# Kernel tuning notes

Hardware: AMD Instinct MI355X
Metric: run time of the kernel (lower is better)

Reference implementation:

```python
import jax, jax.numpy as jnp
import numpy as np

H = 256; HEADS = 4; DH = H // HEADS; LAYERS = 2; FEAT = 7
N = 20000; L = 32; E = 640000


def _ln(x, g, b, eps=1e-5):
    mu = x.mean(-1, keepdims=True)
    var = ((x - mu) ** 2).mean(-1, keepdims=True)
    return (x - mu) / jnp.sqrt(var + eps) * g + b


def setup_inputs() -> dict:
    key = jax.random.key(0)
    ks = jax.random.split(key, 12)
    s = 0.05
    nrm = lambda k, shp: jax.random.normal(k, shp, jnp.float32) * s
    return {
        "literal_reprs": jax.random.normal(ks[0], (N, L, H), jnp.float32),
        "clause_features": jax.random.uniform(ks[1], (N, FEAT), jnp.float32),
        "mask": jax.random.randint(ks[2], (N, L), 0, 2) == 1,
        "adjacency": jax.random.randint(ks[3], (2, E), 0, N),
        "pe_w1": nrm(ks[4], (FEAT, H)), "pe_b1": jnp.zeros((H,), jnp.float32),
        "pe_w2": nrm(ks[5], (H, H)), "pe_b2": jnp.zeros((H,), jnp.float32),
        "attn_in_w": nrm(ks[6], (H, 3 * H)), "attn_in_b": jnp.zeros((3 * H,), jnp.float32),
        "attn_out_w": nrm(ks[7], (H, H)), "attn_out_b": jnp.zeros((H,), jnp.float32),
        "attn_ln_g": jnp.ones((H,), jnp.float32), "attn_ln_b": jnp.zeros((H,), jnp.float32),
        "gate_w": nrm(ks[8], (2 * H, H)), "gate_b": jnp.zeros((H,), jnp.float32),
        "trans_w": nrm(ks[9], (2 * H, H)), "trans_b": jnp.zeros((H,), jnp.float32),
        "fus_ln_g": jnp.ones((H,), jnp.float32), "fus_ln_b": jnp.zeros((H,), jnp.float32),
        "mp_w": nrm(ks[10], (LAYERS, 2 * H, H)), "mp_b": jnp.zeros((LAYERS, H), jnp.float32),
        "mp_ln_g": jnp.ones((LAYERS, H), jnp.float32), "mp_ln_b": jnp.zeros((LAYERS, H), jnp.float32),
    }


def reference(literal_reprs, clause_features, mask, adjacency,
              pe_w1, pe_b1, pe_w2, pe_b2,
              attn_in_w, attn_in_b, attn_out_w, attn_out_b,
              attn_ln_g, attn_ln_b, gate_w, gate_b, trans_w, trans_b,
              fus_ln_g, fus_ln_b, mp_w, mp_b, mp_ln_g, mp_ln_b):
    n, l, h = literal_reprs.shape
    # clause property encoder (shared by query and fusion path)
    enc = jnp.maximum(clause_features @ pe_w1 + pe_b1, 0.0) @ pe_w2 + pe_b2  # (N, H)
    # single-query multi-head attention over literals
    wq, wk, wv = attn_in_w[:, :H], attn_in_w[:, H:2 * H], attn_in_w[:, 2 * H:]
    bq, bk, bv = attn_in_b[:H], attn_in_b[H:2 * H], attn_in_b[2 * H:]
    q = ((enc @ wq + bq) * (1.0 / np.sqrt(DH))).reshape(n, HEADS, DH)
    k = (literal_reprs @ wk + bk).reshape(n, l, HEADS, DH)
    v = (literal_reprs @ wv + bv).reshape(n, l, HEADS, DH)
    scores = jnp.einsum('nhd,nlhd->nhl', q, k)
    kpm = ~mask  # True = masked out
    all_masked = jnp.all(kpm, axis=1)
    kpm = kpm.at[:, 0].set(jnp.where(all_masked, False, kpm[:, 0]))  # unmask pos 0 for fully-masked rows
    scores = jnp.where(kpm[:, None, :], -jnp.inf, scores)
    attn = jax.nn.softmax(scores, axis=-1)
    ctx = jnp.einsum('nhl,nlhd->nhd', attn, v).reshape(n, h) @ attn_out_w + attn_out_b
    ctx = jnp.where(all_masked[:, None], 0.0, ctx)  # zero fully-masked rows
    attn_repr = _ln(ctx + enc, attn_ln_g, attn_ln_b)
    # masked mean-pool residual
    mf = mask.astype(literal_reprs.dtype)[:, :, None]
    lit_mean = (literal_reprs * mf).sum(1) / jnp.maximum(mf.sum(1), 1.0)
    attn_repr = attn_repr + lit_mean
    # gated fusion
    combined = jnp.concatenate([attn_repr, enc], axis=-1)
    gate = jax.nn.sigmoid(combined @ gate_w + gate_b)
    transform = combined @ trans_w + trans_b
    x = _ln(gate * attn_repr + (1.0 - gate) * transform, fus_ln_g, fus_ln_b)
    # inter-clause message passing
    src, dst = adjacency[0], adjacency[1]
    ones = jnp.ones((src.shape[0],), x.dtype)
    for i in range(LAYERS):
        agg = jax.ops.segment_sum(x[src], dst, num_segments=n)
        cnt = jax.ops.segment_sum(ones, dst, num_segments=n)
        agg = agg / jnp.maximum(cnt, 1.0)[:, None]
        upd = jnp.maximum(jnp.concatenate([x, agg], axis=-1) @ mp_w[i] + mp_b[i], 0.0)
        x = _ln(x + upd, mp_ln_g[i], mp_ln_b[i])
    return x
```

## Files before the change

### kernel.cpp

```cpp
#include <hip/hip_runtime.h>
#include <math.h>

#define H 256
#define L 32
#define HEADS 4
#define FEAT 7
#define LN_EPS 1e-5f

typedef __attribute__((ext_vector_type(8))) short bf16x8;
typedef __attribute__((ext_vector_type(4))) float f32x4;

__device__ __forceinline__ float wave_reduce_sum64(float v) {
#pragma unroll
  for (int m = 32; m >= 1; m >>= 1) v += __shfl_xor(v, m, 64);
  return v;
}

__device__ __forceinline__ short bf16rne(float f) {
  unsigned u = __float_as_uint(f);
  unsigned r = (u + 0x7FFFu + ((u >> 16) & 1u)) >> 16;
  return (short)r;
}

__device__ __forceinline__ float bf2f(short s) {
  return __uint_as_float(((unsigned)(unsigned short)s) << 16);
}

__global__ __launch_bounds__(256) void k_pack_w(
    const float* __restrict__ W, short* __restrict__ P, int K, int N) {
  const int KS = K / 32;
  const int total = (N / 16) * KS * 64;
  int t = blockIdx.x * 256 + threadIdx.x;
  if (t >= total) return;
  const int lane = t & 63;
  const int ks = (t >> 6) % KS;
  const int tcol = (t >> 6) / KS;
  const int j = tcol * 16 + (lane & 15);
  const int k0 = ks * 32 + (lane >> 4) * 8;
  short v[8];
#pragma unroll
  for (int i = 0; i < 8; ++i) v[i] = bf16rne(W[(size_t)(k0 + i) * N + j]);
  *(int4*)&P[(size_t)t * 8] = *(int4*)v;
}

__global__ __launch_bounds__(256) void k_pack_w4(
    const float* __restrict__ w0, const float* __restrict__ w1,
    const float* __restrict__ w2, const float* __restrict__ w3,
    short* __restrict__ p0, short* __restrict__ p1,
    short* __restrict__ p2, short* __restrict__ p3) {
  const float* W = (blockIdx.y == 0) ? w0 : (blockIdx.y == 1) ? w1 : (blockIdx.y == 2) ? w2 : w3;
  short* P = (blockIdx.y == 0) ? p0 : (blockIdx.y == 1) ? p1 : (blockIdx.y == 2) ? p2 : p3;
  const int KS = 16;
  int t = blockIdx.x * 256 + threadIdx.x;
  const int lane = t & 63;
  const int ks = (t >> 6) % KS;
  const int tcol = (t >> 6) / KS;
  const int j = tcol * 16 + (lane & 15);
  const int k0 = ks * 32 + (lane >> 4) * 8;
  short v[8];
#pragma unroll
  for (int i = 0; i < 8; ++i) v[i] = bf16rne(W[(size_t)(k0 + i) * 256 + j]);
  *(int4*)&P[(size_t)t * 8] = *(int4*)v;
}

__global__ __launch_bounds__(256) void k_make_wqp(const float* __restrict__ aiw, short* __restrict__ P) {
  int t = blockIdx.x * 256 + threadIdx.x;
  const int lane = t & 63;
  const int ks = (t >> 6) & 7;
  const int tcol = t >> 9;
  const int col = tcol * 16 + (lane & 15);
  const int h = col >> 8, c = col & 255;
  const int k0 = ks * 32 + (lane >> 4) * 8;
  short v[8];
#pragma unroll
  for (int i = 0; i < 8; ++i) {
    const int k = k0 + i;
    float s = 0.f;
    for (int d = 0; d < 64; d += 4) {
      const float4 qa = *(const float4*)&aiw[(size_t)k * 768 + h * 64 + d];
      const float4 ka = *(const float4*)&aiw[(size_t)c * 768 + 256 + h * 64 + d];
      s = fmaf(qa.x, ka.x, fmaf(qa.y, ka.y, fmaf(qa.z, ka.z, fmaf(qa.w, ka.w, s))));
    }
    v[i] = bf16rne(0.125f * s);
  }
  *(int4*)&P[(size_t)t * 8] = *(int4*)v;
}

__global__ __launch_bounds__(256) void k_make_wbig(
    const float* __restrict__ aiw, const float* __restrict__ aow, short* __restrict__ P) {
  int t = blockIdx.x * 256 + threadIdx.x;
  const int lane = t & 63;
  const int ks = (t >> 6) & 31;
  const int tcol = t >> 11;
  const int j = tcol * 16 + (lane & 15);
  const int k0 = ks * 32 + (lane >> 4) * 8;
  short v[8];
#pragma unroll
  for (int i = 0; i < 8; ++i) {
    const int k = k0 + i;
    const int h = k >> 8, c = k & 255;
    float s = 0.f;
    for (int d = 0; d < 64; ++d)
      s = fmaf(aiw[(size_t)c * 768 + 512 + h * 64 + d], aow[(size_t)(h * 64 + d) * 256 + j], s);
    v[i] = bf16rne(s);
  }
  *(int4*)&P[(size_t)t * 8] = *(int4*)v;
}

__global__ void k_bias_p(const float* __restrict__ aiw, const float* __restrict__ aib,
                         float* __restrict__ bias_p) {
  const int col = threadIdx.x + blockIdx.x * 256;
  const int h = col >> 8, c = col & 255;
  float s = 0.f;
  for (int d = 0; d < 64; ++d)
    s = fmaf(aib[h * 64 + d], aiw[(size_t)c * 768 + 256 + h * 64 + d], s);
  bias_p[col] = 0.125f * s;
}

__global__ void k_bias_out(const float* __restrict__ aow, const float* __restrict__ aib,
                           const float* __restrict__ aob, float* __restrict__ bias_out) {
  const int j = threadIdx.x;
  float s = aob[j];
  for (int e = 0; e < 256; ++e) s = fmaf(aib[512 + e], aow[(size_t)e * 256 + j], s);
  bias_out[j] = s;
}

__global__ __launch_bounds__(256) void k_enc_mfma(
    const float* __restrict__ cf, const float* __restrict__ pe_w1, const float* __restrict__ pe_b1,
    const short* __restrict__ w2P, const float* __restrict__ pe_b2,
    const short* __restrict__ wqpP, const float* __restrict__ bias_p,
    short* __restrict__ enc_bf16, short* __restrict__ p_bf16, int n) {
  __shared__ float cfs[32][FEAT];
  __shared__ short h1[32][264];
  __shared__ short encS[32][264];
  const int tid = threadIdx.x;
  const int lane = tid & 63, w = tid >> 6;
  const int n0 = blockIdx.x * 32;
  for (int idx = tid; idx < 32 * FEAT; idx += 256) cfs[idx / FEAT][idx % FEAT] = cf[(size_t)n0 * FEAT + idx];
  __syncthreads();
  {
    const int j = tid;
    float wv[FEAT];
#pragma unroll
    for (int f = 0; f < FEAT; ++f) wv[f] = pe_w1[f * H + j];
    const float b1v = pe_b1[j];
    for (int r = 0; r < 32; ++r) {
      float s = b1v;
#pragma unroll
      for (int f = 0; f < FEAT; ++f) s = fmaf(cfs[r][f], wv[f], s);
      h1[r][j] = bf16rne(fmaxf(s, 0.f));
    }
  }
  __syncthreads();
  const int arow = lane & 15;
  const int koff = (lane >> 4) * 8;
  {
    f32x4 acc[2][4];
#pragma unroll
    for (int rt = 0; rt < 2; ++rt)
#pragma unroll
      for (int ct = 0; ct < 4; ++ct) acc[rt][ct] = (f32x4)0.f;
#pragma unroll
    for (int ks = 0; ks < 8; ++ks) {
      const int k0 = ks * 32 + koff;
      const bf16x8 a0 = *(const bf16x8*)&h1[arow][k0];
      const bf16x8 a1 = *(const bf16x8*)&h1[16 + arow][k0];
#pragma unroll
      for (int ct = 0; ct < 4; ++ct) {
        const size_t fo = (((size_t)(w * 4 + ct) * 8 + ks) * 64 + lane) * 8;
        const bf16x8 b = *(const bf16x8*)&w2P[fo];
        acc[0][ct] = __builtin_amdgcn_mfma_f32_16x16x32_bf16(a0, b, acc[0][ct], 0, 0, 0);
        acc[1][ct] = __builtin_amdgcn_mfma_f32_16x16x32_bf16(a1, b, acc[1][ct], 0, 0, 0);
      }
    }
#pragma unroll
    for (int rt = 0; rt < 2; ++rt)
#pragma unroll
      for (int ct = 0; ct < 4; ++ct) {
        const int col = w * 64 + ct * 16 + (lane & 15);
        const float b2v = pe_b2[col];
#pragma unroll
        for (int i = 0; i < 4; ++i) {
          const int row = rt * 16 + (lane >> 4) * 4 + i;
          const short bv = bf16rne(acc[rt][ct][i] + b2v);
          encS[row][col] = bv;
          enc_bf16[(size_t)(n0 + row) * H + col] = bv;
        }
      }
  }
  __syncthreads();
#pragma unroll
  for (int chunk = 0; chunk < 2; ++chunk) {
    f32x4 acc[2][8];
#pragma unroll
    for (int rt = 0; rt < 2; ++rt)
#pragma unroll
      for (int c8 = 0; c8 < 8; ++c8) acc[rt][c8] = (f32x4)0.f;
#pragma unroll
    for (int ks = 0; ks < 8; ++ks) {
      const int k0 = ks * 32 + koff;
      const bf16x8 a0 = *(const bf16x8*)&encS[arow][k0];
      const bf16x8 a1 = *(const bf16x8*)&encS[16 + arow][k0];
#pragma unroll
      for (int c8 = 0; c8 < 8; ++c8) {
        const int tcol = w * 16 + chunk * 8 + c8;
        const size_t fo = (((size_t)tcol * 8 + ks) * 64 + lane) * 8;
        const bf16x8 b = *(const bf16x8*)&wqpP[fo];
        acc[0][c8] = __builtin_amdgcn_mfma_f32_16x16x32_bf16(a0, b, acc[0][c8], 0, 0, 0);
        acc[1][c8] = __builtin_amdgcn_mfma_f32_16x16x32_bf16(a1, b, acc[1][c8], 0, 0, 0);
      }
    }
#pragma unroll
    for (int rt = 0; rt < 2; ++rt)
#pragma unroll
      for (int c8 = 0; c8 < 8; ++c8) {
        const int col = w * 256 + (chunk * 8 + c8) * 16 + (lane & 15);
        const float bp = bias_p[col];
#pragma unroll
        for (int i = 0; i < 4; ++i) {
          const int row = rt * 16 + (lane >> 4) * 4 + i;
          p_bf16[(size_t)(n0 + row) * 1024 + col] = bf16rne(acc[rt][c8][i] + bp);
        }
      }
  }
}

__global__ __launch_bounds__(256) void k_attn(
    const float* __restrict__ lit, const int* __restrict__ mask,
    const short* __restrict__ p_in, short* __restrict__ m_out,
    short* __restrict__ litmean_bf, int* __restrict__ flags, int n) {
  __shared__ short lit_bs[32][264];
  __shared__ float attn_s[32][4];
  __shared__ int validS[32];
  __shared__ int nvalidS;
  const int j = threadIdx.x;
  const int nn = blockIdx.x;
  const float* litrow = lit + (size_t)nn * (L * H);
  float lreg[32];
#pragma unroll
  for (int t = 0; t < 32; ++t) {
    const float v = litrow[t * 256 + j];
    lreg[t] = v;
    lit_bs[t][j] = bf16rne(v);
  }
  if (j < 32) validS[j] = (mask[(size_t)nn * L + j] != 0) ? 1 : 0;
  __syncthreads();
  if (j == 0) {
    int c = 0;
#pragma unroll
    for (int l = 0; l < 32; ++l) c += validS[l];
    nvalidS = c;
  }
  __syncthreads();
  const int nvalid = nvalidS;
  const bool allm = (nvalid == 0);
  if (j < 64) {
    const int lane = j;
    f32x4 sc0 = (f32x4)0.f, sc1 = (f32x4)0.f;
    const int hh = lane & 3;
    const int krow = (lane >> 4) * 8;
    const short* prow = p_in + (size_t)nn * 1024 + hh * 256;
#pragma unroll
    for (int ks = 0; ks < 8; ++ks) {
      const bf16x8 a = *(const bf16x8*)&prow[ks * 32 + krow];
      const bf16x8 b0 = *(const bf16x8*)&lit_bs[lane & 15][ks * 32 + krow];
      const bf16x8 b1 = *(const bf16x8*)&lit_bs[16 + (lane & 15)][ks * 32 + krow];
      sc0 = __builtin_amdgcn_mfma_f32_16x16x32_bf16(a, b0, sc0, 0, 0, 0);
      sc1 = __builtin_amdgcn_mfma_f32_16x16x32_bf16(a, b1, sc1, 0, 0, 0);
    }
    if (lane < 16) {
      const int l0 = lane, l1 = 16 + lane;
      const bool ok0 = validS[l0] || (allm && l0 == 0);
      const bool ok1 = validS[l1] != 0;
#pragma unroll
      for (int i = 0; i < 4; ++i) {
        float s0 = ok0 ? sc0[i] : -INFINITY;
        float s1 = ok1 ? sc1[i] : -INFINITY;
        float mx = fmaxf(s0, s1);
#pragma unroll
        for (int m = 8; m >= 1; m >>= 1) mx = fmaxf(mx, __shfl_xor(mx, m, 16));
        float e0 = ok0 ? __expf(s0 - mx) : 0.f;
        float e1 = ok1 ? __expf(s1 - mx) : 0.f;
        float sm = e0 + e1;
#pragma unroll
        for (int m = 8; m >= 1; m >>= 1) sm += __shfl_xor(sm, m, 16);
        const float inv = 1.f / sm;
        attn_s[l0][i] = e0 * inv;
        attn_s[l1][i] = e1 * inv;
      }
    }
  }
  __syncthreads();
  {
    const float inv = 1.f / fmaxf((float)nvalid, 1.f);
    float lm = 0.f;
#pragma unroll
    for (int l = 0; l < 32; ++l)
      if (validS[l]) lm += lreg[l];
    litmean_bf[(size_t)nn * H + j] = bf16rne(lm * inv);
    float mm0 = 0.f, mm1 = 0.f, mm2 = 0.f, mm3 = 0.f;
#pragma unroll
    for (int l = 0; l < 32; ++l) {
      const float4 av = *(const float4*)&attn_s[l][0];
      const float lv = lreg[l];
      mm0 = fmaf(av.x, lv, mm0);
      mm1 = fmaf(av.y, lv, mm1);
      mm2 = fmaf(av.z, lv, mm2);
      mm3 = fmaf(av.w, lv, mm3);
    }
    m_out[(size_t)nn * 1024 + 0 * 256 + j] = bf16rne(mm0);
    m_out[(size_t)nn * 1024 + 1 * 256 + j] = bf16rne(mm1);
    m_out[(size_t)nn * 1024 + 2 * 256 + j] = bf16rne(mm2);
    m_out[(size_t)nn * 1024 + 3 * 256 + j] = bf16rne(mm3);
  }
  if (j == 0) flags[nn] = allm ? 1 : 0;
}

__global__ __launch_bounds__(256) void k_fused(
    const short* __restrict__ m_bf16, const short* __restrict__ wbigP, const float* __restrict__ bias_out,
    const short* __restrict__ enc_bf16, const short* __restrict__ litmean_bf, const int* __restrict__ flags,
    const float* __restrict__ ag, const float* __restrict__ ab,
    const short* __restrict__ gwP, const short* __restrict__ twP,
    const float* __restrict__ gb, const float* __restrict__ tb,
    const float* __restrict__ fg, const float* __restrict__ fb,
    short* __restrict__ xout_bf, int n) {
  __shared__ short As[32][520];
  __shared__ float v_s[32][260];
  __shared__ float mu_s[32], sg_s[32];
  __shared__ int flagS[32];
  const int tid = threadIdx.x;
  const int lane = tid & 63, w = tid >> 6;
  const int n0 = blockIdx.x * 32;
  for (int q8 = tid; q8 < 32 * 32; q8 += 256) {
    const int idx = q8 << 3;
    const int r = idx >> 8, c = idx & 255;
    *(int4*)&As[r][256 + c] = *(const int4*)&enc_bf16[(size_t)(n0 + r) * H + c];
  }
  if (tid < 32) flagS[tid] = flags[n0 + tid];
  const int arow = lane & 15;
  const int koff = (lane >> 4) * 8;
  f32x4 acc[2][4];
#pragma unroll
  for (int rt = 0; rt < 2; ++rt)
#pragma unroll
    for (int ct = 0; ct < 4; ++ct) acc[rt][ct] = (f32x4)0.f;
#pragma unroll 8
  for (int ks = 0; ks < 32; ++ks) {
    const size_t abase = (size_t)(n0 + arow) * 1024 + ks * 32 + koff;
    const bf16x8 a0 = *(const bf16x8*)&m_bf16[abase];
    const bf16x8 a1 = *(const bf16x8*)&m_bf16[abase + 16 * 1024];
#pragma unroll
    for (int ct = 0; ct < 4; ++ct) {
      const size_t fo = (((size_t)(w * 4 + ct) * 32 + ks) * 64 + lane) * 8;
      const bf16x8 bw = *(const bf16x8*)&wbigP[fo];
      acc[0][ct] = __builtin_amdgcn_mfma_f32_16x16x32_bf16(a0, bw, acc[0][ct], 0, 0, 0);
      acc[1][ct] = __builtin_amdgcn_mfma_f32_16x16x32_bf16(a1, bw, acc[1][ct], 0, 0, 0);
    }
  }
  __syncthreads();
#pragma unroll
  for (int rt = 0; rt < 2; ++rt)
#pragma unroll
    for (int ct = 0; ct < 4; ++ct) {
      const int col = w * 64 + ct * 16 + (lane & 15);
      const float bo = bias_out[col];
#pragma unroll
      for (int i = 0; i < 4; ++i) {
        const int row = rt * 16 + (lane >> 4) * 4 + i;
        const float o = flagS[row] ? 0.f : (acc[rt][ct][i] + bo);
        v_s[row][col] = o + bf2f(As[row][256 + col]);
      }
    }
  __syncthreads();
  for (int r = w; r < 32; r += 4) {
    float ps = 0.f, pq = 0.f;
#pragma unroll
    for (int t = 0; t < 4; ++t) {
      float v = v_s[r][lane + 64 * t];
      ps += v;
      pq = fmaf(v, v, pq);
    }
    ps = wave_reduce_sum64(ps);
    pq = wave_reduce_sum64(pq);
    if (lane == 0) {
      float mu = ps * (1.f / H);
      mu_s[r] = mu;
      sg_s[r] = rsqrtf(pq * (1.f / H) - mu * mu + LN_EPS);
    }
  }
  __syncthreads();
  {
    const float agv = ag[tid], abv = ab[tid];
    for (int r = 0; r < 32; ++r) {
      const float val = (v_s[r][tid] - mu_s[r]) * sg_s[r] * agv + abv +
                        bf2f(litmean_bf[(size_t)(n0 + r) * H + tid]);
      As[r][tid] = bf16rne(val);
    }
  }
  __syncthreads();
  f32x4 accg[2][4], acct[2][4];
#pragma unroll
  for (int rt = 0; rt < 2; ++rt)
#pragma unroll
    for (int ct = 0; ct < 4; ++ct) { accg[rt][ct] = (f32x4)0.f; acct[rt][ct] = (f32x4)0.f; }
#pragma unroll 4
  for (int ks = 0; ks < 16; ++ks) {
    const int k0 = ks * 32 + koff;
    const bf16x8 a0 = *(const bf16x8*)&As[arow][k0];
    const bf16x8 a1 = *(const bf16x8*)&As[16 + arow][k0];
#pragma unroll
    for (int ct = 0; ct < 4; ++ct) {
      const size_t fo = (((size_t)(w * 4 + ct) * 16 + ks) * 64 + lane) * 8;
      const bf16x8 bg = *(const bf16x8*)&gwP[fo];
      const bf16x8 bt = *(const bf16x8*)&twP[fo];
      accg[0][ct] = __builtin_amdgcn_mfma_f32_16x16x32_bf16(a0, bg, accg[0][ct], 0, 0, 0);
      accg[1][ct] = __builtin_amdgcn_mfma_f32_16x16x32_bf16(a1, bg, accg[1][ct], 0, 0, 0);
      acct[0][ct] = __builtin_amdgcn_mfma_f32_16x16x32_bf16(a0, bt, acct[0][ct], 0, 0, 0);
      acct[1][ct] = __builtin_amdgcn_mfma_f32_16x16x32_bf16(a1, bt, acct[1][ct], 0, 0, 0);
    }
  }
#pragma unroll
  for (int rt = 0; rt < 2; ++rt)
#pragma unroll
    for (int ct = 0; ct < 4; ++ct) {
      const int col = w * 64 + ct * 16 + (lane & 15);
      const float gbv = gb[col], tbv = tb[col];
#pragma unroll
      for (int i = 0; i < 4; ++i) {
        const int rl = rt * 16 + (lane >> 4) * 4 + i;
        const float gate = 1.f / (1.f + __expf(-(accg[rt][ct][i] + gbv)));
        const float tr = acct[rt][ct][i] + tbv;
        const float a = bf2f(As[rl][col]);
        v_s[rl][col] = fmaf(gate, a - tr, tr);
      }
    }
  __syncthreads();
  for (int r = w; r < 32; r += 4) {
    float ps = 0.f, pq = 0.f;
#pragma unroll
    for (int t = 0; t < 4; ++t) {
      float v = v_s[r][lane + 64 * t];
      ps += v;
      pq = fmaf(v, v, pq);
    }
    ps = wave_reduce_sum64(ps);
    pq = wave_reduce_sum64(pq);
    if (lane == 0) {
      float mu = ps * (1.f / H);
      mu_s[r] = mu;
      sg_s[r] = rsqrtf(pq * (1.f / H) - mu * mu + LN_EPS);
    }
  }
  __syncthreads();
  {
    const float fgv = fg[tid], fbv = fb[tid];
    for (int r = 0; r < 32; ++r)
      xout_bf[(size_t)(n0 + r) * H + tid] = bf16rne((v_s[r][tid] - mu_s[r]) * sg_s[r] * fgv + fbv);
  }
}

__global__ __launch_bounds__(256) void k_mp_mfma(
    const short* __restrict__ xin_bf, const short* __restrict__ agg_bf,
    const short* __restrict__ wP, const float* __restrict__ bias,
    const float* __restrict__ g, const float* __restrict__ b,
    float* __restrict__ xout_f32, short* __restrict__ xout_bf, int n) {
  __shared__ short As[32][520];
  __shared__ float v_s[32][260];
  __shared__ float mu_s[32], sg_s[32];
  const int tid = threadIdx.x;
  const int lane = tid & 63, w = tid >> 6;
  const int n0 = blockIdx.x * 32;
  for (int q8 = tid; q8 < 32 * 64; q8 += 256) {
    const int idx = q8 << 3;
    const int r = idx >> 9, c = idx & 511;
    const short* src = (c < H) ? &xin_bf[(size_t)(n0 + r) * H + c]
                               : &agg_bf[(size_t)(n0 + r) * H + (c - H)];
    *(int4*)&As[r][c] = *(const int4*)src;
  }
  __syncthreads();
  f32x4 acc[2][4];
#pragma unroll
  for (int rt = 0; rt < 2; ++rt)
#pragma unroll
    for (int ct = 0; ct < 4; ++ct) acc[rt][ct] = (f32x4)0.f;
  const int arow = lane & 15;
  const int koff = (lane >> 4) * 8;
#pragma unroll 4
  for (int ks = 0; ks < 16; ++ks) {
    const int k0 = ks * 32 + koff;
    const bf16x8 a0 = *(const bf16x8*)&As[arow][k0];
    const bf16x8 a1 = *(const bf16x8*)&As[16 + arow][k0];
#pragma unroll
    for (int ct = 0; ct < 4; ++ct) {
      const size_t fo = (((size_t)(w * 4 + ct) * 16 + ks) * 64 + lane) * 8;
      const bf16x8 bw = *(const bf16x8*)&wP[fo];
      acc[0][ct] = __builtin_amdgcn_mfma_f32_16x16x32_bf16(a0, bw, acc[0][ct], 0, 0, 0);
      acc[1][ct] = __builtin_amdgcn_mfma_f32_16x16x32_bf16(a1, bw, acc[1][ct], 0, 0, 0);
    }
  }
#pragma unroll
  for (int rt = 0; rt < 2; ++rt)
#pragma unroll
    for (int ct = 0; ct < 4; ++ct) {
      const int col = w * 64 + ct * 16 + (lane & 15);
      const float bsv = bias[col];
#pragma unroll
      for (int i = 0; i < 4; ++i) {
        const int rl = rt * 16 + (lane >> 4) * 4 + i;
        const float u = fmaxf(acc[rt][ct][i] + bsv, 0.f);
        v_s[rl][col] = bf2f(As[rl][col]) + u;
      }
    }
  __syncthreads();
  for (int r = w; r < 32; r += 4) {
    float ps = 0.f, pq = 0.f;
#pragma unroll
    for (int t = 0; t < 4; ++t) {
      float v = v_s[r][lane + 64 * t];
      ps += v;
      pq = fmaf(v, v, pq);
    }
    ps = wave_reduce_sum64(ps);
    pq = wave_reduce_sum64(pq);
    if (lane == 0) {
      float mu = ps * (1.f / H);
      mu_s[r] = mu;
      sg_s[r] = rsqrtf(pq * (1.f / H) - mu * mu + LN_EPS);
    }
  }
  __syncthreads();
  const float gv = g[tid], bv = b[tid];
  for (int r = 0; r < 32; ++r) {
    const float val = (v_s[r][tid] - mu_s[r]) * sg_s[r] * gv + bv;
    if (xout_f32) xout_f32[(size_t)(n0 + r) * H + tid] = val;
    if (xout_bf) xout_bf[(size_t)(n0 + r) * H + tid] = bf16rne(val);
  }
}

__global__ void k_zero_int(int* __restrict__ p, int count) {
  int i = blockIdx.x * blockDim.x + threadIdx.x;
  if (i < count) p[i] = 0;
}

__global__ void k_hist(const int* __restrict__ dst, int* __restrict__ hist, int e) {
  int i = blockIdx.x * blockDim.x + threadIdx.x;
  if (i < e) atomicAdd(&hist[dst[i]], 1);
}

__global__ __launch_bounds__(1024) void k_scan(
    const int* __restrict__ hist, int* __restrict__ row_ptr, int* __restrict__ cursor, int n, int e) {
  __shared__ int part[1024];
  const int t = threadIdx.x;
  const int chunk = (n + 1023) / 1024;
  const int lo = t * chunk;
  const int hi = min(lo + chunk, n);
  int s = 0;
  for (int i = lo; i < hi; ++i) s += hist[i];
  part[t] = s;
  __syncthreads();
  for (int d = 1; d < 1024; d <<= 1) {
    int v = (t >= d) ? part[t - d] : 0;
    __syncthreads();
    part[t] += v;
    __syncthreads();
  }
  int run = (t > 0) ? part[t - 1] : 0;
  for (int i = lo; i < hi; ++i) {
    row_ptr[i] = run;
    cursor[i] = run;
    run += hist[i];
  }
  if (t == 1023) row_ptr[n] = e;
}

__global__ void k_fill(const int* __restrict__ adj, int* __restrict__ cursor,
                       int* __restrict__ edge_src, int e) {
  int i = blockIdx.x * blockDim.x + threadIdx.x;
  if (i < e) {
    int s = adj[i], d = adj[e + i];
    int pos = atomicAdd(&cursor[d], 1);
    edge_src[pos] = s;
  }
}

__global__ __launch_bounds__(256) void k_gather(
    const short* __restrict__ x, const int* __restrict__ edge_src, const int* __restrict__ row_ptr,
    short* __restrict__ agg, int n) {
  const int wid = threadIdx.x >> 6;
  const int lane = threadIdx.x & 63;
  const int d = blockIdx.x * 4 + wid;
  if (d >= n) return;
  const int beg = row_ptr[d], end = row_ptr[d + 1];
  float4 acc = {0.f, 0.f, 0.f, 0.f};
  int i = beg;
  for (; i + 4 <= end; i += 4) {
    const int s0 = edge_src[i], s1 = edge_src[i + 1], s2 = edge_src[i + 2], s3 = edge_src[i + 3];
    const short4 v0 = *(const short4*)(x + (size_t)s0 * H + lane * 4);
    const short4 v1 = *(const short4*)(x + (size_t)s1 * H + lane * 4);
    const short4 v2 = *(const short4*)(x + (size_t)s2 * H + lane * 4);
    const short4 v3 = *(const short4*)(x + (size_t)s3 * H + lane * 4);
    acc.x += bf2f(v0.x) + bf2f(v1.x) + bf2f(v2.x) + bf2f(v3.x);
    acc.y += bf2f(v0.y) + bf2f(v1.y) + bf2f(v2.y) + bf2f(v3.y);
    acc.z += bf2f(v0.z) + bf2f(v1.z) + bf2f(v2.z) + bf2f(v3.z);
    acc.w += bf2f(v0.w) + bf2f(v1.w) + bf2f(v2.w) + bf2f(v3.w);
  }
  for (; i < end; ++i) {
    const int s = edge_src[i];
    const short4 v = *(const short4*)(x + (size_t)s * H + lane * 4);
    acc.x += bf2f(v.x); acc.y += bf2f(v.y); acc.z += bf2f(v.z); acc.w += bf2f(v.w);
  }
  const float inv = 1.f / fmaxf((float)(end - beg), 1.f);
  short4 o;
  o.x = bf16rne(acc.x * inv); o.y = bf16rne(acc.y * inv);
  o.z = bf16rne(acc.z * inv); o.w = bf16rne(acc.w * inv);
  *(short4*)(agg + (size_t)d * H + lane * 4) = o;
}

extern "C" void kernel_launch(void* const* d_in, const int* in_sizes, int n_in,
                              void* d_out, int out_size, void* d_ws, size_t ws_size,
                              hipStream_t stream) {
  const float* lit = (const float*)d_in[0];
  const float* cf = (const float*)d_in[1];
  const int* mask = (const int*)d_in[2];
  const int* adj = (const int*)d_in[3];
  const float* pe_w1 = (const float*)d_in[4];
  const float* pe_b1 = (const float*)d_in[5];
  const float* pe_w2 = (const float*)d_in[6];
  const float* pe_b2 = (const float*)d_in[7];
  const float* aiw = (const float*)d_in[8];
  const float* aib = (const float*)d_in[9];
  const float* aow = (const float*)d_in[10];
  const float* aob = (const float*)d_in[11];
  const float* attn_ln_g = (const float*)d_in[12];
  const float* attn_ln_b = (const float*)d_in[13];
  const float* gate_w = (const float*)d_in[14];
  const float* gate_b = (const float*)d_in[15];
  const float* trans_w = (const float*)d_in[16];
  const float* trans_b = (const float*)d_in[17];
  const float* fus_ln_g = (const float*)d_in[18];
  const float* fus_ln_b = (const float*)d_in[19];
  const float* mp_w = (const float*)d_in[20];
  const float* mp_b = (const float*)d_in[21];
  const float* mp_ln_g = (const float*)d_in[22];
  const float* mp_ln_b = (const float*)d_in[23];

  const int n = in_sizes[1] / FEAT;
  const int e = in_sizes[3] / 2;

  float* ws = (float*)d_ws;
  size_t off = 0;
  short* enc_bf16 = (short*)(ws + off); off += (size_t)n * 128;
  short* pm_bf16 = (short*)(ws + off); off += (size_t)n * 512;
  short* litmean_bf = (short*)(ws + off); off += (size_t)n * 128;
  short* x0_bf = (short*)(ws + off); off += (size_t)n * 128;
  short* x1_bf = (short*)(ws + off); off += (size_t)n * 128;
  short* agg_bf = (short*)(ws + off); off += (size_t)n * 128;
  int* flags = (int*)(ws + off); off += n;
  int* hist = (int*)(ws + off); off += n;
  int* row_ptr = (int*)(ws + off); off += n + 2;
  int* cursor = (int*)(ws + off); off += n;
  int* edge_src = (int*)(ws + off); off += e;
  short* w2P = (short*)(ws + off); off += 256 * 256 / 2;
  short* wqpP = (short*)(ws + off); off += 256 * 1024 / 2;
  short* wbigP = (short*)(ws + off); off += 1024 * 256 / 2;
  short* gwP = (short*)(ws + off); off += 512 * 256 / 2;
  short* twP = (short*)(ws + off); off += 512 * 256 / 2;
  short* mp0P = (short*)(ws + off); off += 512 * 256 / 2;
  short* mp1P = (short*)(ws + off); off += 512 * 256 / 2;
  float* bias_p = ws + off; off += 1024;
  float* bias_out = ws + off; off += 256;

  dim3 blk(256);
  k_pack_w<<<32, blk, 0, stream>>>(pe_w2, w2P, 256, 256);
  k_pack_w4<<<dim3(64, 4), blk, 0, stream>>>(gate_w, trans_w, mp_w, mp_w + 512 * 256,
                                             gwP, twP, mp0P, mp1P);
  k_make_wqp<<<128, blk, 0, stream>>>(aiw, wqpP);
  k_make_wbig<<<128, blk, 0, stream>>>(aiw, aow, wbigP);
  k_bias_p<<<4, blk, 0, stream>>>(aiw, aib, bias_p);
  k_bias_out<<<1, blk, 0, stream>>>(aow, aib, aob, bias_out);

  k_enc_mfma<<<n / 32, blk, 0, stream>>>(cf, pe_w1, pe_b1, w2P, pe_b2, wqpP, bias_p, enc_bf16, pm_bf16, n);
  k_attn<<<n, blk, 0, stream>>>(lit, mask, pm_bf16, pm_bf16, litmean_bf, flags, n);

  k_zero_int<<<(n + 255) / 256, blk, 0, stream>>>(hist, n);
  k_hist<<<(e + 255) / 256, blk, 0, stream>>>(adj + e, hist, e);
  k_scan<<<1, 1024, 0, stream>>>(hist, row_ptr, cursor, n, e);
  k_fill<<<(e + 255) / 256, blk, 0, stream>>>(adj, cursor, edge_src, e);

  k_fused<<<n / 32, blk, 0, stream>>>(pm_bf16, wbigP, bias_out, enc_bf16, litmean_bf, flags,
                                      attn_ln_g, attn_ln_b, gwP, twP, gate_b, trans_b,
                                      fus_ln_g, fus_ln_b, x0_bf, n);
  k_gather<<<(n + 3) / 4, blk, 0, stream>>>(x0_bf, edge_src, row_ptr, agg_bf, n);
  k_mp_mfma<<<n / 32, blk, 0, stream>>>(x0_bf, agg_bf, mp0P, mp_b, mp_ln_g, mp_ln_b,
                                        nullptr, x1_bf, n);
  k_gather<<<(n + 3) / 4, blk, 0, stream>>>(x1_bf, edge_src, row_ptr, agg_bf, n);
  k_mp_mfma<<<n / 32, blk, 0, stream>>>(x1_bf, agg_bf, mp1P, mp_b + 256, mp_ln_g + 256, mp_ln_b + 256,
                                        (float*)d_out, nullptr, n);
}
```

Baseline: 657.5 us.

## Fuse neighbor gather into MP GEMM, merge prep kernels, vectorize attention loads

The six weight-prep launches are merged into one block-dispatched k_prep kernel. The per-layer k_gather kernel is removed: each k_mp_mfma block now computes the mean over its rows' incoming neighbors straight into shared memory, which drops the agg buffer's global write and read. k_attn now loads literals as float4 into bf16 shared memory instead of keeping fp32 copies in registers. It also writes the per-head context vector interleaved (j*4+h) with a single short4 store, and the wbig packing layout is changed to match. The literal mean is now computed from bf16-rounded values, which slightly lowers its precision, and the fused gather puts irregular latency inside the GEMM blocks.

```diff
diff --git a/kernel.cpp b/kernel.cpp
--- a/kernel.cpp
+++ b/kernel.cpp
@@ -26,103 +26,93 @@
   return __uint_as_float(((unsigned)(unsigned short)s) << 16);
 }
 
-__global__ __launch_bounds__(256) void k_pack_w(
-    const float* __restrict__ W, short* __restrict__ P, int K, int N) {
-  const int KS = K / 32;
-  const int total = (N / 16) * KS * 64;
-  int t = blockIdx.x * 256 + threadIdx.x;
-  if (t >= total) return;
-  const int lane = t & 63;
-  const int ks = (t >> 6) % KS;
-  const int tcol = (t >> 6) / KS;
-  const int j = tcol * 16 + (lane & 15);
-  const int k0 = ks * 32 + (lane >> 4) * 8;
-  short v[8];
-#pragma unroll
-  for (int i = 0; i < 8; ++i) v[i] = bf16rne(W[(size_t)(k0 + i) * N + j]);
-  *(int4*)&P[(size_t)t * 8] = *(int4*)v;
-}
-
-__global__ __launch_bounds__(256) void k_pack_w4(
-    const float* __restrict__ w0, const float* __restrict__ w1,
-    const float* __restrict__ w2, const float* __restrict__ w3,
-    short* __restrict__ p0, short* __restrict__ p1,
-    short* __restrict__ p2, short* __restrict__ p3) {
-  const float* W = (blockIdx.y == 0) ? w0 : (blockIdx.y == 1) ? w1 : (blockIdx.y == 2) ? w2 : w3;
-  short* P = (blockIdx.y == 0) ? p0 : (blockIdx.y == 1) ? p1 : (blockIdx.y == 2) ? p2 : p3;
-  const int KS = 16;
-  int t = blockIdx.x * 256 + threadIdx.x;
-  const int lane = t & 63;
-  const int ks = (t >> 6) % KS;
-  const int tcol = (t >> 6) / KS;
-  const int j = tcol * 16 + (lane & 15);
-  const int k0 = ks * 32 + (lane >> 4) * 8;
-  short v[8];
-#pragma unroll
-  for (int i = 0; i < 8; ++i) v[i] = bf16rne(W[(size_t)(k0 + i) * 256 + j]);
-  *(int4*)&P[(size_t)t * 8] = *(int4*)v;
-}
-
-__global__ __launch_bounds__(256) void k_make_wqp(const float* __restrict__ aiw, short* __restrict__ P) {
-  int t = blockIdx.x * 256 + threadIdx.x;
-  const int lane = t & 63;
-  const int ks = (t >> 6) & 7;
-  const int tcol = t >> 9;
-  const int col = tcol * 16 + (lane & 15);
-  const int h = col >> 8, c = col & 255;
-  const int k0 = ks * 32 + (lane >> 4) * 8;
-  short v[8];
-#pragma unroll
-  for (int i = 0; i < 8; ++i) {
-    const int k = k0 + i;
-    float s = 0.f;
-    for (int d = 0; d < 64; d += 4) {
-      const float4 qa = *(const float4*)&aiw[(size_t)k * 768 + h * 64 + d];
-      const float4 ka = *(const float4*)&aiw[(size_t)c * 768 + 256 + h * 64 + d];
-      s = fmaf(qa.x, ka.x, fmaf(qa.y, ka.y, fmaf(qa.z, ka.z, fmaf(qa.w, ka.w, s))));
-    }
-    v[i] = bf16rne(0.125f * s);
-  }
-  *(int4*)&P[(size_t)t * 8] = *(int4*)v;
-}
-
-__global__ __launch_bounds__(256) void k_make_wbig(
-    const float* __restrict__ aiw, const float* __restrict__ aow, short* __restrict__ P) {
-  int t = blockIdx.x * 256 + threadIdx.x;
-  const int lane = t & 63;
-  const int ks = (t >> 6) & 31;
-  const int tcol = t >> 11;
-  const int j = tcol * 16 + (lane & 15);
-  const int k0 = ks * 32 + (lane >> 4) * 8;
-  short v[8];
-#pragma unroll
-  for (int i = 0; i < 8; ++i) {
-    const int k = k0 + i;
-    const int h = k >> 8, c = k & 255;
+__global__ __launch_bounds__(256) void k_prep(
+    const float* __restrict__ pe_w2, const float* __restrict__ aiw, const float* __restrict__ aow,
+    const float* __restrict__ aib, const float* __restrict__ aob,
+    const float* __restrict__ gate_w, const float* __restrict__ trans_w, const float* __restrict__ mp_w,
+    short* __restrict__ w2P, short* __restrict__ wqpP, short* __restrict__ wbigP,
+    short* __restrict__ gwP, short* __restrict__ twP, short* __restrict__ mp0P, short* __restrict__ mp1P,
+    float* __restrict__ bias_p, float* __restrict__ bias_out) {
+  const int bb = blockIdx.x;
+  const int tid = threadIdx.x;
+  if (bb < 32) {
+    const int t = bb * 256 + tid;
+    const int lane = t & 63;
+    const int ks = (t >> 6) & 7;
+    const int tcol = (t >> 6) >> 3;
+    const int j = tcol * 16 + (lane & 15);
+    const int k0 = ks * 32 + (lane >> 4) * 8;
+    short v[8];
+#pragma unroll
+    for (int i = 0; i < 8; ++i) v[i] = bf16rne(pe_w2[(size_t)(k0 + i) * 256 + j]);
+    *(int4*)&w2P[(size_t)t * 8] = *(int4*)v;
+  } else if (bb < 160) {
+    const int t = (bb - 32) * 256 + tid;
+    const int lane = t & 63;
+    const int ks = (t >> 6) & 7;
+    const int tcol = t >> 9;
+    const int col = tcol * 16 + (lane & 15);
+    const int h = col >> 8, c = col & 255;
+    const int k0 = ks * 32 + (lane >> 4) * 8;
+    short v[8];
+#pragma unroll
+    for (int i = 0; i < 8; ++i) {
+      const int k = k0 + i;
+      float s = 0.f;
+      for (int d = 0; d < 64; d += 4) {
+        const float4 qa = *(const float4*)&aiw[(size_t)k * 768 + h * 64 + d];
+        const float4 ka = *(const float4*)&aiw[(size_t)c * 768 + 256 + h * 64 + d];
+        s = fmaf(qa.x, ka.x, fmaf(qa.y, ka.y, fmaf(qa.z, ka.z, fmaf(qa.w, ka.w, s))));
+      }
+      v[i] = bf16rne(0.125f * s);
+    }
+    *(int4*)&wqpP[(size_t)t * 8] = *(int4*)v;
+  } else if (bb < 288) {
+    const int t = (bb - 160) * 256 + tid;
+    const int lane = t & 63;
+    const int ks = (t >> 6) & 31;
+    const int tcol = t >> 11;
+    const int j = tcol * 16 + (lane & 15);
+    const int k0 = ks * 32 + (lane >> 4) * 8;
+    short v[8];
+#pragma unroll
+    for (int i = 0; i < 8; ++i) {
+      const int k = k0 + i;
+      const int c = k >> 2, h = k & 3;
+      float s = 0.f;
+      for (int d = 0; d < 64; ++d)
+        s = fmaf(aiw[(size_t)c * 768 + 512 + h * 64 + d], aow[(size_t)(h * 64 + d) * 256 + j], s);
+      v[i] = bf16rne(s);
+    }
+    *(int4*)&wbigP[(size_t)t * 8] = *(int4*)v;
+  } else if (bb < 544) {
+    const int sub = bb - 288;
+    const int mi = sub >> 6;
+    const float* W = (mi == 0) ? gate_w : (mi == 1) ? trans_w : (mi == 2) ? mp_w : (mp_w + 512 * 256);
+    short* P = (mi == 0) ? gwP : (mi == 1) ? twP : (mi == 2) ? mp0P : mp1P;
+    const int t = (sub & 63) * 256 + tid;
+    const int lane = t & 63;
+    const int ks = (t >> 6) & 15;
+    const int tcol = (t >> 6) >> 4;
+    const int j = tcol * 16 + (lane & 15);
+    const int k0 = ks * 32 + (lane >> 4) * 8;
+    short v[8];
+#pragma unroll
+    for (int i = 0; i < 8; ++i) v[i] = bf16rne(W[(size_t)(k0 + i) * 256 + j]);
+    *(int4*)&P[(size_t)t * 8] = *(int4*)v;
+  } else if (bb < 548) {
+    const int col = (bb - 544) * 256 + tid;
+    const int h = col >> 8, c = col & 255;
     float s = 0.f;
     for (int d = 0; d < 64; ++d)
-      s = fmaf(aiw[(size_t)c * 768 + 512 + h * 64 + d], aow[(size_t)(h * 64 + d) * 256 + j], s);
-    v[i] = bf16rne(s);
-  }
-  *(int4*)&P[(size_t)t * 8] = *(int4*)v;
-}
-
-__global__ void k_bias_p(const float* __restrict__ aiw, const float* __restrict__ aib,
-                         float* __restrict__ bias_p) {
-  const int col = threadIdx.x + blockIdx.x * 256;
-  const int h = col >> 8, c = col & 255;
-  float s = 0.f;
-  for (int d = 0; d < 64; ++d)
-    s = fmaf(aib[h * 64 + d], aiw[(size_t)c * 768 + 256 + h * 64 + d], s);
-  bias_p[col] = 0.125f * s;
-}
-
-__global__ void k_bias_out(const float* __restrict__ aow, const float* __restrict__ aib,
-                           const float* __restrict__ aob, float* __restrict__ bias_out) {
-  const int j = threadIdx.x;
-  float s = aob[j];
-  for (int e = 0; e < 256; ++e) s = fmaf(aib[512 + e], aow[(size_t)e * 256 + j], s);
-  bias_out[j] = s;
+      s = fmaf(aib[h * 64 + d], aiw[(size_t)c * 768 + 256 + h * 64 + d], s);
+    bias_p[col] = 0.125f * s;
+  } else {
+    const int j = tid;
+    float s = aob[j];
+    for (int e2 = 0; e2 < 256; ++e2) s = fmaf(aib[512 + e2], aow[(size_t)e2 * 256 + j], s);
+    bias_out[j] = s;
+  }
 }
 
 __global__ __launch_bounds__(256) void k_enc_mfma(
@@ -236,12 +226,14 @@
   const int j = threadIdx.x;
   const int nn = blockIdx.x;
   const float* litrow = lit + (size_t)nn * (L * H);
-  float lreg[32];
-#pragma unroll
-  for (int t = 0; t < 32; ++t) {
-    const float v = litrow[t * 256 + j];
-    lreg[t] = v;
-    lit_bs[t][j] = bf16rne(v);
+#pragma unroll
+  for (int t = 0; t < 8; ++t) {
+    const int idx = (t * 256 + j) << 2;
+    const int r = idx >> 8, c = idx & 255;
+    const float4 f = *(const float4*)&litrow[idx];
+    short4 hv;
+    hv.x = bf16rne(f.x); hv.y = bf16rne(f.y); hv.z = bf16rne(f.z); hv.w = bf16rne(f.w);
+    *(short4*)&lit_bs[r][c] = hv;
   }
   if (j < 32) validS[j] = (mask[(size_t)nn * L + j] != 0) ? 1 : 0;
   __syncthreads();
@@ -294,24 +286,21 @@
   {
     const float inv = 1.f / fmaxf((float)nvalid, 1.f);
     float lm = 0.f;
-#pragma unroll
-    for (int l = 0; l < 32; ++l)
-      if (validS[l]) lm += lreg[l];
-    litmean_bf[(size_t)nn * H + j] = bf16rne(lm * inv);
     float mm0 = 0.f, mm1 = 0.f, mm2 = 0.f, mm3 = 0.f;
 #pragma unroll
     for (int l = 0; l < 32; ++l) {
+      const float lv = bf2f(lit_bs[l][j]);
+      if (validS[l]) lm += lv;
       const float4 av = *(const float4*)&attn_s[l][0];
-      const float lv = lreg[l];
       mm0 = fmaf(av.x, lv, mm0);
       mm1 = fmaf(av.y, lv, mm1);
       mm2 = fmaf(av.z, lv, mm2);
       mm3 = fmaf(av.w, lv, mm3);
     }
-    m_out[(size_t)nn * 1024 + 0 * 256 + j] = bf16rne(mm0);
-    m_out[(size_t)nn * 1024 + 1 * 256 + j] = bf16rne(mm1);
-    m_out[(size_t)nn * 1024 + 2 * 256 + j] = bf16rne(mm2);
-    m_out[(size_t)nn * 1024 + 3 * 256 + j] = bf16rne(mm3);
+    litmean_bf[(size_t)nn * H + j] = bf16rne(lm * inv);
+    short4 mv;
+    mv.x = bf16rne(mm0); mv.y = bf16rne(mm1); mv.z = bf16rne(mm2); mv.w = bf16rne(mm3);
+    *(short4*)&m_out[(size_t)nn * 1024 + j * 4] = mv;
   }
   if (j == 0) flags[nn] = allm ? 1 : 0;
 }
@@ -460,7 +449,7 @@
 }
 
 __global__ __launch_bounds__(256) void k_mp_mfma(
-    const short* __restrict__ xin_bf, const short* __restrict__ agg_bf,
+    const short* __restrict__ xin_bf, const int* __restrict__ edge_src, const int* __restrict__ row_ptr,
     const short* __restrict__ wP, const float* __restrict__ bias,
     const float* __restrict__ g, const float* __restrict__ b,
     float* __restrict__ xout_f32, short* __restrict__ xout_bf, int n) {
@@ -470,12 +459,37 @@
   const int tid = threadIdx.x;
   const int lane = tid & 63, w = tid >> 6;
   const int n0 = blockIdx.x * 32;
-  for (int q8 = tid; q8 < 32 * 64; q8 += 256) {
+  for (int q8 = tid; q8 < 32 * 32; q8 += 256) {
     const int idx = q8 << 3;
-    const int r = idx >> 9, c = idx & 511;
-    const short* src = (c < H) ? &xin_bf[(size_t)(n0 + r) * H + c]
-                               : &agg_bf[(size_t)(n0 + r) * H + (c - H)];
-    *(int4*)&As[r][c] = *(const int4*)src;
+    const int r = idx >> 8, c = idx & 255;
+    *(int4*)&As[r][c] = *(const int4*)&xin_bf[(size_t)(n0 + r) * H + c];
+  }
+  for (int rr = w; rr < 32; rr += 4) {
+    const int d = n0 + rr;
+    const int beg = row_ptr[d], end = row_ptr[d + 1];
+    float4 acc = {0.f, 0.f, 0.f, 0.f};
+    int i = beg;
+    for (; i + 4 <= end; i += 4) {
+      const int s0 = edge_src[i], s1 = edge_src[i + 1], s2 = edge_src[i + 2], s3 = edge_src[i + 3];
+      const short4 v0 = *(const short4*)(xin_bf + (size_t)s0 * H + lane * 4);
+      const short4 v1 = *(const short4*)(xin_bf + (size_t)s1 * H + lane * 4);
+      const short4 v2 = *(const short4*)(xin_bf + (size_t)s2 * H + lane * 4);
+      const short4 v3 = *(const short4*)(xin_bf + (size_t)s3 * H + lane * 4);
+      acc.x += bf2f(v0.x) + bf2f(v1.x) + bf2f(v2.x) + bf2f(v3.x);
+      acc.y += bf2f(v0.y) + bf2f(v1.y) + bf2f(v2.y) + bf2f(v3.y);
+      acc.z += bf2f(v0.z) + bf2f(v1.z) + bf2f(v2.z) + bf2f(v3.z);
+      acc.w += bf2f(v0.w) + bf2f(v1.w) + bf2f(v2.w) + bf2f(v3.w);
+    }
+    for (; i < end; ++i) {
+      const int s = edge_src[i];
+      const short4 v = *(const short4*)(xin_bf + (size_t)s * H + lane * 4);
+      acc.x += bf2f(v.x); acc.y += bf2f(v.y); acc.z += bf2f(v.z); acc.w += bf2f(v.w);
+    }
+    const float inv = 1.f / fmaxf((float)(end - beg), 1.f);
+    short4 o;
+    o.x = bf16rne(acc.x * inv); o.y = bf16rne(acc.y * inv);
+    o.z = bf16rne(acc.z * inv); o.w = bf16rne(acc.w * inv);
+    *(short4*)&As[rr][256 + lane * 4] = o;
   }
   __syncthreads();
   f32x4 acc[2][4];
@@ -581,39 +595,6 @@
     int pos = atomicAdd(&cursor[d], 1);
     edge_src[pos] = s;
   }
-}
-
-__global__ __launch_bounds__(256) void k_gather(
-    const short* __restrict__ x, const int* __restrict__ edge_src, const int* __restrict__ row_ptr,
-    short* __restrict__ agg, int n) {
-  const int wid = threadIdx.x >> 6;
-  const int lane = threadIdx.x & 63;
-  const int d = blockIdx.x * 4 + wid;
-  if (d >= n) return;
-  const int beg = row_ptr[d], end = row_ptr[d + 1];
-  float4 acc = {0.f, 0.f, 0.f, 0.f};
-  int i = beg;
-  for (; i + 4 <= end; i += 4) {
-    const int s0 = edge_src[i], s1 = edge_src[i + 1], s2 = edge_src[i + 2], s3 = edge_src[i + 3];
-    const short4 v0 = *(const short4*)(x + (size_t)s0 * H + lane * 4);
-    const short4 v1 = *(const short4*)(x + (size_t)s1 * H + lane * 4);
-    const short4 v2 = *(const short4*)(x + (size_t)s2 * H + lane * 4);
-    const short4 v3 = *(const short4*)(x + (size_t)s3 * H + lane * 4);
-    acc.x += bf2f(v0.x) + bf2f(v1.x) + bf2f(v2.x) + bf2f(v3.x);
-    acc.y += bf2f(v0.y) + bf2f(v1.y) + bf2f(v2.y) + bf2f(v3.y);
-    acc.z += bf2f(v0.z) + bf2f(v1.z) + bf2f(v2.z) + bf2f(v3.z);
-    acc.w += bf2f(v0.w) + bf2f(v1.w) + bf2f(v2.w) + bf2f(v3.w);
-  }
-  for (; i < end; ++i) {
-    const int s = edge_src[i];
-    const short4 v = *(const short4*)(x + (size_t)s * H + lane * 4);
-    acc.x += bf2f(v.x); acc.y += bf2f(v.y); acc.z += bf2f(v.z); acc.w += bf2f(v.w);
-  }
-  const float inv = 1.f / fmaxf((float)(end - beg), 1.f);
-  short4 o;
-  o.x = bf16rne(acc.x * inv); o.y = bf16rne(acc.y * inv);
-  o.z = bf16rne(acc.z * inv); o.w = bf16rne(acc.w * inv);
-  *(short4*)(agg + (size_t)d * H + lane * 4) = o;
 }
 
 extern "C" void kernel_launch(void* const* d_in, const int* in_sizes, int n_in,
@@ -654,7 +635,6 @@
   short* litmean_bf = (short*)(ws + off); off += (size_t)n * 128;
   short* x0_bf = (short*)(ws + off); off += (size_t)n * 128;
   short* x1_bf = (short*)(ws + off); off += (size_t)n * 128;
-  short* agg_bf = (short*)(ws + off); off += (size_t)n * 128;
   int* flags = (int*)(ws + off); off += n;
   int* hist = (int*)(ws + off); off += n;
   int* row_ptr = (int*)(ws + off); off += n + 2;
@@ -671,13 +651,8 @@
   float* bias_out = ws + off; off += 256;
 
   dim3 blk(256);
-  k_pack_w<<<32, blk, 0, stream>>>(pe_w2, w2P, 256, 256);
-  k_pack_w4<<<dim3(64, 4), blk, 0, stream>>>(gate_w, trans_w, mp_w, mp_w + 512 * 256,
-                                             gwP, twP, mp0P, mp1P);
-  k_make_wqp<<<128, blk, 0, stream>>>(aiw, wqpP);
-  k_make_wbig<<<128, blk, 0, stream>>>(aiw, aow, wbigP);
-  k_bias_p<<<4, blk, 0, stream>>>(aiw, aib, bias_p);
-  k_bias_out<<<1, blk, 0, stream>>>(aow, aib, aob, bias_out);
+  k_prep<<<549, blk, 0, stream>>>(pe_w2, aiw, aow, aib, aob, gate_w, trans_w, mp_w,
+                                  w2P, wqpP, wbigP, gwP, twP, mp0P, mp1P, bias_p, bias_out);
 
   k_enc_mfma<<<n / 32, blk, 0, stream>>>(cf, pe_w1, pe_b1, w2P, pe_b2, wqpP, bias_p, enc_bf16, pm_bf16, n);
   k_attn<<<n, blk, 0, stream>>>(lit, mask, pm_bf16, pm_bf16, litmean_bf, flags, n);
@@ -690,10 +665,8 @@
   k_fused<<<n / 32, blk, 0, stream>>>(pm_bf16, wbigP, bias_out, enc_bf16, litmean_bf, flags,
                                       attn_ln_g, attn_ln_b, gwP, twP, gate_b, trans_b,
                                       fus_ln_g, fus_ln_b, x0_bf, n);
-  k_gather<<<(n + 3) / 4, blk, 0, stream>>>(x0_bf, edge_src, row_ptr, agg_bf, n);
-  k_mp_mfma<<<n / 32, blk, 0, stream>>>(x0_bf, agg_bf, mp0P, mp_b, mp_ln_g, mp_ln_b,
+  k_mp_mfma<<<n / 32, blk, 0, stream>>>(x0_bf, edge_src, row_ptr, mp0P, mp_b, mp_ln_g, mp_ln_b,
                                         nullptr, x1_bf, n);
-  k_gather<<<(n + 3) / 4, blk, 0, stream>>>(x1_bf, edge_src, row_ptr, agg_bf, n);
-  k_mp_mfma<<<n / 32, blk, 0, stream>>>(x1_bf, agg_bf, mp1P, mp_b + 256, mp_ln_g + 256, mp_ln_b + 256,
-                                        (float*)d_out, nullptr, n);
-}
+  k_mp_mfma<<<n / 32, blk, 0, stream>>>(x1_bf, edge_src, row_ptr, mp1P, mp_b + 256, mp_ln_g + 256,
+                                        mp_ln_b + 256, (float*)d_out, nullptr, n);
+}
```

Result: slower. 724.8 us (+10.2%).
